# Kernel optimization log

Hardware: AMD Instinct MI355X
Metric: run time of the kernel (lower is better)

## Reference

```python
import jax, jax.numpy as jnp
import numpy as np

N = 50000   # nodes
E = 800000  # edges (sparse adjacency nnz)
FI = 256    # input feature dim
FO = 64     # output feature dim per head
H = 8       # attention heads


def setup_inputs() -> dict:
    key = jax.random.key(0)
    ks = jax.random.split(key, 6)
    x = jax.random.normal(ks[0], (N, FI), dtype=jnp.float32)
    W = jax.random.normal(ks[1], (H, FI, FO), dtype=jnp.float32) * 0.05
    a = jax.random.normal(ks[2], (H, FO), dtype=jnp.float32) * 0.05
    b = jax.random.normal(ks[3], (H, FO), dtype=jnp.float32) * 0.05
    rows = jax.random.randint(ks[4], (E,), 0, N, dtype=jnp.int32)
    cols = jax.random.randint(ks[5], (E,), 0, N, dtype=jnp.int32)
    return {"x": x, "W": W, "a": a, "b": b, "rows": rows, "cols": cols}


def reference(x, W, a, b, rows, cols):
    # SparseGAT forward: per head linear -> edge scores -> sparse row softmax
    # -> sparse aggregation -> bias; heads averaged then ReLU.
    n = x.shape[0]
    h = W.shape[0]
    NEG_SLOPE = 0.2  # tf.nn.leaky_relu default alpha
    acc = None
    for i in range(h):  # small fixed loop over heads
        t = x @ W[i]                                   # [N, FO]
        aw = t @ a[i]                                  # [N]
        e = jax.nn.leaky_relu(aw[rows] + aw[cols], NEG_SLOPE)   # [E]
        # sparse softmax per row (segment softmax, numerically stable)
        m = jax.ops.segment_max(e, rows, num_segments=n)        # [N]
        ex = jnp.exp(e - m[rows])                                # [E]
        den = jax.ops.segment_sum(ex, rows, num_segments=n)      # [N]
        coef = ex / den[rows]                                    # [E]
        # sparse matmul: sum_j coef_ij * t_j
        agg = jax.ops.segment_sum(coef[:, None] * t[cols], rows, num_segments=n)
        agg = agg + b[i]
        acc = agg if acc is None else acc + agg
    return jax.nn.relu(acc / h)
```

## Files before the change

kernel.cpp:

```cpp
#include <hip/hip_runtime.h>
#include <hip/hip_bf16.h>


#define FI 256
#define FO 64
#define NH 8
#define FC 512
#define BM 128

typedef _Float16 f16x8 __attribute__((ext_vector_type(8)));
typedef float f32x16 __attribute__((ext_vector_type(16)));
typedef float f32x8 __attribute__((ext_vector_type(8)));
typedef float f32x4 __attribute__((ext_vector_type(4)));

__global__ __launch_bounds__(256)
void p1_wconv(const float* __restrict__ W, _Float16* __restrict__ Wth) {
  int idx = blockIdx.x * 256 + threadIdx.x;
  if (idx >= NH * FO * FI) return;
  int k = idx & (FI - 1);
  int f = (idx >> 8) & (FO - 1);
  int h = idx >> 14;
  Wth[idx] = (_Float16)W[((size_t)h * FI + k) * FO + f];
}

__global__ __launch_bounds__(512)
void k1_v2(const float* __restrict__ x, const _Float16* __restrict__ Wth,
           const float* __restrict__ a, _Float16* __restrict__ Th2,
           float* __restrict__ aw, int N) {
  __shared__ _Float16 smem[BM * 136];
  auto Xs = reinterpret_cast<_Float16(*)[136]>(smem);
  auto Tt = reinterpret_cast<_Float16(*)[512]>(smem);
  const int bm = blockIdx.x * BM;
  const int t = threadIdx.x;
  const int w = t >> 6;
  const int lane = t & 63;
  const int l31 = lane & 31;
  const int kh = (lane >> 5) * 8;
  const _Float16* Wh = Wth + (size_t)w * (FO * FI);

  f32x16 acc[4][2];
  #pragma unroll
  for (int mr = 0; mr < 4; ++mr)
    #pragma unroll
    for (int wc = 0; wc < 2; ++wc) acc[mr][wc] = (f32x16)0.0f;

  #pragma unroll
  for (int k0 = 0; k0 < 2; ++k0) {
    if (k0) __syncthreads();
    #pragma unroll
    for (int r = 0; r < 8; ++r) {
      int i = t + r * 512;
      int row = i >> 5;
      int q = i & 31;
      float4 v = make_float4(0.f, 0.f, 0.f, 0.f);
      if (bm + row < N)
        v = reinterpret_cast<const float4*>(&x[(size_t)(bm + row) * FI + k0 * 128])[q];
      _Float16 o[4] = {(_Float16)v.x, (_Float16)v.y, (_Float16)v.z, (_Float16)v.w};
      *reinterpret_cast<uint2*>(&Xs[row][q * 4]) = *reinterpret_cast<uint2*>(o);
    }
    __syncthreads();
    #pragma unroll
    for (int kk = 0; kk < 8; ++kk) {
      f16x8 af[4], bf[2];
      #pragma unroll
      for (int mr = 0; mr < 4; ++mr)
        af[mr] = *reinterpret_cast<const f16x8*>(&Xs[mr * 32 + l31][kk * 16 + kh]);
      #pragma unroll
      for (int wc = 0; wc < 2; ++wc)
        bf[wc] = *reinterpret_cast<const f16x8*>(
            &Wh[(size_t)(wc * 32 + l31) * FI + k0 * 128 + kk * 16 + kh]);
      #pragma unroll
      for (int mr = 0; mr < 4; ++mr)
        #pragma unroll
        for (int wc = 0; wc < 2; ++wc)
          acc[mr][wc] =
              __builtin_amdgcn_mfma_f32_32x32x16_f16(af[mr], bf[wc], acc[mr][wc], 0, 0, 0);
    }
  }

  const float av0 = a[w * FO + l31], av1 = a[w * FO + 32 + l31];
  #pragma unroll
  for (int mr = 0; mr < 4; ++mr)
    #pragma unroll
    for (int reg = 0; reg < 16; ++reg) {
      float s = acc[mr][0][reg] * av0 + acc[mr][1][reg] * av1;
      #pragma unroll
      for (int off = 1; off < 32; off <<= 1) s += __shfl_xor(s, off);
      if (l31 == 0) {
        int rl = mr * 32 + (reg & 3) + 8 * (reg >> 2) + 4 * (lane >> 5);
        if (bm + rl < N) aw[(size_t)(bm + rl) * NH + w] = s;
      }
    }

  #pragma unroll
  for (int ch = 0; ch < 4; ++ch) {
    __syncthreads();
    #pragma unroll
    for (int wc = 0; wc < 2; ++wc) {
      const int f = wc * 32 + l31;
      #pragma unroll
      for (int reg = 0; reg < 16; ++reg) {
        int rl = (reg & 3) + 8 * (reg >> 2) + 4 * (lane >> 5);
        Tt[rl][f * NH + w] = (_Float16)acc[ch][wc][reg];
      }
    }
    __syncthreads();
    #pragma unroll
    for (int r = 0; r < 4; ++r) {
      int i = t + r * 512;
      int row = i >> 6, q = i & 63;
      int grow = bm + ch * 32 + row;
      if (grow < N)
        *reinterpret_cast<uint4*>(&Th2[(size_t)grow * FC + q * 8]) =
            *reinterpret_cast<const uint4*>(&Tt[row][q * 8]);
    }
  }
}

__global__ __launch_bounds__(256)
void b1_hist(const int* __restrict__ rows, int* __restrict__ deg, int E) {
  int e = blockIdx.x * 256 + threadIdx.x;
  if (e < E) atomicAdd(&deg[rows[e]], 1);
}

__global__ __launch_bounds__(256)
void b2a_blocksum(const int* __restrict__ deg, int* __restrict__ blocksums, int N) {
  __shared__ int red[256];
  const int t = threadIdx.x;
  const int base = blockIdx.x * 1024 + t * 4;
  int s = 0;
  #pragma unroll
  for (int j = 0; j < 4; ++j) { int i = base + j; if (i < N) s += deg[i]; }
  red[t] = s;
  __syncthreads();
  for (int off = 128; off; off >>= 1) {
    if (t < off) red[t] += red[t + off];
    __syncthreads();
  }
  if (t == 0) blocksums[blockIdx.x] = red[0];
}

__global__ __launch_bounds__(64)
void b2b_scanblocks(int* __restrict__ blocksums, int nb,
                    int* __restrict__ row_start, int N, int E) {
  const int lane = threadIdx.x;
  int carry = 0;
  for (int base = 0; base < nb; base += 64) {
    int i = base + lane;
    int v = (i < nb) ? blocksums[i] : 0;
    int inc = v;
    #pragma unroll
    for (int off = 1; off < 64; off <<= 1) {
      int t = __shfl_up(inc, off);
      if (lane >= off) inc += t;
    }
    if (i < nb) blocksums[i] = inc - v + carry;
    carry += __shfl(inc, 63);
  }
  if (lane == 0) row_start[N] = E;
}

__global__ __launch_bounds__(256)
void b2c_rescan(const int* __restrict__ deg, const int* __restrict__ blocksums,
                int* __restrict__ row_start, int* __restrict__ cursor, int N) {
  __shared__ int ts[256];
  const int t = threadIdx.x;
  const int base = blockIdx.x * 1024 + t * 4;
  int v[4]; int s = 0;
  #pragma unroll
  for (int j = 0; j < 4; ++j) { int i = base + j; v[j] = (i < N) ? deg[i] : 0; s += v[j]; }
  ts[t] = s;
  __syncthreads();
  for (int off = 1; off < 256; off <<= 1) {
    int add = (t >= off) ? ts[t - off] : 0;
    __syncthreads();
    ts[t] += add;
    __syncthreads();
  }
  int run = blocksums[blockIdx.x] + ts[t] - s;
  #pragma unroll
  for (int j = 0; j < 4; ++j) {
    int i = base + j;
    if (i < N) { row_start[i] = run; cursor[i] = run; run += v[j]; }
  }
}

__global__ __launch_bounds__(256)
void b3_scatter(const int* __restrict__ rows, const int* __restrict__ cols,
                int* __restrict__ cursor, int* __restrict__ colperm, int E) {
  int e = blockIdx.x * 256 + threadIdx.x;
  if (e >= E) return;
  int pos = atomicAdd(&cursor[rows[e]], 1);
  colperm[pos] = cols[e];
}

__global__ __launch_bounds__(256)
void k4_fused(const int* __restrict__ row_start, const int* __restrict__ colperm,
              const float* __restrict__ aw, const _Float16* __restrict__ Th2,
              const float* __restrict__ b, float* __restrict__ out, int N) {
  __shared__ float exs[16][132];
  const int lane16 = threadIdx.x & 15;
  const int g      = threadIdx.x >> 4;
  const int gbase  = threadIdx.x & 48;
  const int r = blockIdx.x * 16 + g;
  if (r >= N) return;
  float* exg = &exs[g][0];

  const int s0 = row_start[r], s1 = row_start[r + 1];
  f32x8 awr = *reinterpret_cast<const f32x8*>(&aw[(size_t)r * NH]);

  float facc[4][NH] = {};
  float dacc[NH] = {};

  for (int base = s0; base < s1; base += 16) {
    const int mm = min(16, s1 - base);
    const bool valid = lane16 < mm;
    int c_l = valid ? colperm[base + lane16] : 0;

    f32x8 awc = *reinterpret_cast<const f32x8*>(&aw[(size_t)c_l * NH]);
    #pragma unroll
    for (int h = 0; h < NH; ++h) {
      float s = awr[h] + awc[h];
      float lr = s > 0.f ? s : 0.2f * s;
      float e = valid ? __expf(lr) : 0.f;
      dacc[h] += e;
      exg[lane16 * NH + h] = e;
    }

    int cj = __shfl(c_l, gbase);
    const _Float16* tp = Th2 + (size_t)cj * FC + lane16 * NH;
    f16x8 A0 = *reinterpret_cast<const f16x8*>(tp);
    f16x8 A1 = *reinterpret_cast<const f16x8*>(tp + 128);
    f16x8 A2 = *reinterpret_cast<const f16x8*>(tp + 256);
    f16x8 A3 = *reinterpret_cast<const f16x8*>(tp + 384);
    for (int j = 0; j < mm; ++j) {
      f16x8 B0, B1, B2, B3;
      if (j + 1 < mm) {
        int cn = __shfl(c_l, gbase + j + 1);
        const _Float16* tq = Th2 + (size_t)cn * FC + lane16 * NH;
        B0 = *reinterpret_cast<const f16x8*>(tq);
        B1 = *reinterpret_cast<const f16x8*>(tq + 128);
        B2 = *reinterpret_cast<const f16x8*>(tq + 256);
        B3 = *reinterpret_cast<const f16x8*>(tq + 384);
      }
      f32x4 e0 = *reinterpret_cast<const f32x4*>(&exg[j * NH]);
      f32x4 e1 = *reinterpret_cast<const f32x4*>(&exg[j * NH + 4]);
      #pragma unroll
      for (int h = 0; h < 4; ++h) {
        facc[0][h]     = fmaf(e0[h], (float)A0[h],     facc[0][h]);
        facc[1][h]     = fmaf(e0[h], (float)A1[h],     facc[1][h]);
        facc[2][h]     = fmaf(e0[h], (float)A2[h],     facc[2][h]);
        facc[3][h]     = fmaf(e0[h], (float)A3[h],     facc[3][h]);
        facc[0][h + 4] = fmaf(e1[h], (float)A0[h + 4], facc[0][h + 4]);
        facc[1][h + 4] = fmaf(e1[h], (float)A1[h + 4], facc[1][h + 4]);
        facc[2][h + 4] = fmaf(e1[h], (float)A2[h + 4], facc[2][h + 4]);
        facc[3][h + 4] = fmaf(e1[h], (float)A3[h + 4], facc[3][h + 4]);
      }
      A0 = B0; A1 = B1; A2 = B2; A3 = B3;
    }
  }

  #pragma unroll
  for (int h = 0; h < NH; ++h) {
    #pragma unroll
    for (int off = 1; off < 16; off <<= 1)
      dacc[h] += __shfl_xor(dacc[h], off);
  }

  float rden[NH];
  #pragma unroll
  for (int h = 0; h < NH; ++h) rden[h] = dacc[h] > 0.f ? 1.0f / dacc[h] : 0.f;

  #pragma unroll
  for (int q = 0; q < 4; ++q) {
    const int f = q * 16 + lane16;
    float sb = 0.f;
    #pragma unroll
    for (int h = 0; h < NH; ++h) sb += b[h * FO + f];
    float v = 0.f;
    #pragma unroll
    for (int h = 0; h < NH; ++h) v += facc[q][h] * rden[h];
    v = (v + sb) * 0.125f;
    out[(size_t)r * FO + f] = v > 0.f ? v : 0.f;
  }
}

extern "C" void kernel_launch(void* const* d_in, const int* in_sizes, int n_in,
                              void* d_out, int out_size, void* d_ws, size_t ws_size,
                              hipStream_t stream) {
  const float* x    = (const float*)d_in[0];
  const float* W    = (const float*)d_in[1];
  const float* a    = (const float*)d_in[2];
  const float* b    = (const float*)d_in[3];
  const int*   rows = (const int*)d_in[4];
  const int*   cols = (const int*)d_in[5];
  const int N = in_sizes[0] / FI;
  const int E = in_sizes[4];

  char* p = (char*)d_ws;
  _Float16* Th2      = (_Float16*)p;  p += (size_t)N * FC * sizeof(_Float16);
  _Float16* Wth      = (_Float16*)p;  p += (size_t)NH * FO * FI * sizeof(_Float16);
  float*    aw       = (float*)p;     p += (size_t)N * NH * sizeof(float);
  int*      deg      = (int*)p;       p += (size_t)N * sizeof(int);
  int*      row_start= (int*)p;       p += (size_t)(N + 4) * sizeof(int);
  int*      cursor   = (int*)p;       p += (size_t)N * sizeof(int);
  int*      colperm  = (int*)p;       p += (size_t)E * sizeof(int);
  int*      blocksums= (int*)p;       p += 64 * sizeof(int);
  float*    out = (float*)d_out;

  const int nb = (N + 1023) / 1024;

  hipMemsetAsync(deg, 0, (size_t)N * sizeof(int), stream);
  b1_hist<<<(E + 255) / 256, 256, 0, stream>>>(rows, deg, E);
  b2a_blocksum<<<nb, 256, 0, stream>>>(deg, blocksums, N);
  b2b_scanblocks<<<1, 64, 0, stream>>>(blocksums, nb, row_start, N, E);
  b2c_rescan<<<nb, 256, 0, stream>>>(deg, blocksums, row_start, cursor, N);
  b3_scatter<<<(E + 255) / 256, 256, 0, stream>>>(rows, cols, cursor, colperm, E);

  p1_wconv<<<(NH * FO * FI + 255) / 256, 256, 0, stream>>>(W, Wth);
  k1_v2<<<(N + BM - 1) / BM, 512, 0, stream>>>(x, Wth, a, Th2, aw, N);

  k4_fused<<<(N + 15) / 16, 256, 0, stream>>>(row_start, colperm, aw, Th2, b, out, N);
}
```

Baseline: 292.6 us.

## Pipeline two neighbor rows per step, keep edge weights in registers via shuffles

The aggregation kernel now keeps the attention exponentials in registers, packs them as half2 and broadcasts them with shuffles, so the shared-memory staging buffer is gone. The inner gather loop prefetches two neighbor feature rows per iteration instead of one, which doubles memory-level parallelism. The kernel also becomes a grid-stride loop over 16-row tiles with half as many blocks. In exchange it uses more registers for the doubled buffers, adds shuffle traffic, and rounds the softmax numerators to fp16 before accumulation.

```diff
diff --git a/kernel.cpp b/kernel.cpp
--- a/kernel.cpp
+++ b/kernel.cpp
@@ -1,5 +1,6 @@
 #include <hip/hip_runtime.h>
 #include <hip/hip_bf16.h>
+#include <hip/hip_fp16.h>
 
 
 #define FI 256
@@ -198,90 +199,118 @@
 void k4_fused(const int* __restrict__ row_start, const int* __restrict__ colperm,
               const float* __restrict__ aw, const _Float16* __restrict__ Th2,
               const float* __restrict__ b, float* __restrict__ out, int N) {
-  __shared__ float exs[16][132];
   const int lane16 = threadIdx.x & 15;
-  const int g      = threadIdx.x >> 4;
   const int gbase  = threadIdx.x & 48;
-  const int r = blockIdx.x * 16 + g;
-  if (r >= N) return;
-  float* exg = &exs[g][0];
-
-  const int s0 = row_start[r], s1 = row_start[r + 1];
-  f32x8 awr = *reinterpret_cast<const f32x8*>(&aw[(size_t)r * NH]);
-
-  float facc[4][NH] = {};
-  float dacc[NH] = {};
-
-  for (int base = s0; base < s1; base += 16) {
-    const int mm = min(16, s1 - base);
-    const bool valid = lane16 < mm;
-    int c_l = valid ? colperm[base + lane16] : 0;
-
-    f32x8 awc = *reinterpret_cast<const f32x8*>(&aw[(size_t)c_l * NH]);
+  const int ntiles = (N + 15) / 16;
+
+  for (int tile = blockIdx.x; tile < ntiles; tile += gridDim.x) {
+    const int r = tile * 16 + (threadIdx.x >> 4);
+    if (r >= N) continue;
+
+    const int s0 = row_start[r], s1 = row_start[r + 1];
+    f32x8 awr = *reinterpret_cast<const f32x8*>(&aw[(size_t)r * NH]);
+
+    float facc[4][NH] = {};
+    float dacc[NH] = {};
+
+    for (int base = s0; base < s1; base += 16) {
+      const int mm = min(16, s1 - base);
+      const bool valid = lane16 < mm;
+      int c_l = valid ? colperm[base + lane16] : 0;
+
+      f32x8 awc = *reinterpret_cast<const f32x8*>(&aw[(size_t)c_l * NH]);
+      float ex[NH];
+      uint32_t pk[4];
+      #pragma unroll
+      for (int h = 0; h < NH; ++h) {
+        float s = awr[h] + awc[h];
+        float lr = s > 0.f ? s : 0.2f * s;
+        ex[h] = valid ? __expf(lr) : 0.f;
+        dacc[h] += ex[h];
+      }
+      #pragma unroll
+      for (int q = 0; q < 4; ++q) {
+        __half2 h2 = __floats2half2_rn(ex[2 * q], ex[2 * q + 1]);
+        pk[q] = *reinterpret_cast<uint32_t*>(&h2);
+      }
+
+      f16x8 A0[4], A1[4], B0[4], B1[4];
+      {
+        int c0 = __shfl(c_l, gbase + 0);
+        int c1 = __shfl(c_l, gbase + 1);
+        const _Float16* t0 = Th2 + (size_t)c0 * FC + lane16 * NH;
+        const _Float16* t1 = Th2 + (size_t)c1 * FC + lane16 * NH;
+        #pragma unroll
+        for (int q = 0; q < 4; ++q) {
+          A0[q] = *reinterpret_cast<const f16x8*>(t0 + q * 128);
+          A1[q] = *reinterpret_cast<const f16x8*>(t1 + q * 128);
+        }
+      }
+      for (int j = 0; j < mm; j += 2) {
+        if (j + 2 < mm) {
+          int c0 = __shfl(c_l, gbase + j + 2);
+          int c1 = __shfl(c_l, gbase + j + 3);
+          const _Float16* t0 = Th2 + (size_t)c0 * FC + lane16 * NH;
+          const _Float16* t1 = Th2 + (size_t)c1 * FC + lane16 * NH;
+          #pragma unroll
+          for (int q = 0; q < 4; ++q) {
+            B0[q] = *reinterpret_cast<const f16x8*>(t0 + q * 128);
+            B1[q] = *reinterpret_cast<const f16x8*>(t1 + q * 128);
+          }
+        }
+        float e0[NH], e1[NH];
+        #pragma unroll
+        for (int q = 0; q < 4; ++q) {
+          int p = __shfl((int)pk[q], gbase + j);
+          float2 f2 = __half22float2(*reinterpret_cast<__half2*>(&p));
+          e0[2 * q] = f2.x; e0[2 * q + 1] = f2.y;
+        }
+        #pragma unroll
+        for (int q = 0; q < 4; ++q) {
+          int p = __shfl((int)pk[q], gbase + j + 1);
+          float2 f2 = __half22float2(*reinterpret_cast<__half2*>(&p));
+          e1[2 * q] = f2.x; e1[2 * q + 1] = f2.y;
+        }
+        #pragma unroll
+        for (int q = 0; q < 4; ++q)
+          #pragma unroll
+          for (int h = 0; h < NH; ++h)
+            facc[q][h] = fmaf(e0[h], (float)A0[q][h], facc[q][h]);
+        if (j + 1 < mm) {
+          #pragma unroll
+          for (int q = 0; q < 4; ++q)
+            #pragma unroll
+            for (int h = 0; h < NH; ++h)
+              facc[q][h] = fmaf(e1[h], (float)A1[q][h], facc[q][h]);
+        }
+        #pragma unroll
+        for (int q = 0; q < 4; ++q) { A0[q] = B0[q]; A1[q] = B1[q]; }
+      }
+    }
+
     #pragma unroll
     for (int h = 0; h < NH; ++h) {
-      float s = awr[h] + awc[h];
-      float lr = s > 0.f ? s : 0.2f * s;
-      float e = valid ? __expf(lr) : 0.f;
-      dacc[h] += e;
-      exg[lane16 * NH + h] = e;
-    }
-
-    int cj = __shfl(c_l, gbase);
-    const _Float16* tp = Th2 + (size_t)cj * FC + lane16 * NH;
-    f16x8 A0 = *reinterpret_cast<const f16x8*>(tp);
-    f16x8 A1 = *reinterpret_cast<const f16x8*>(tp + 128);
-    f16x8 A2 = *reinterpret_cast<const f16x8*>(tp + 256);
-    f16x8 A3 = *reinterpret_cast<const f16x8*>(tp + 384);
-    for (int j = 0; j < mm; ++j) {
-      f16x8 B0, B1, B2, B3;
-      if (j + 1 < mm) {
-        int cn = __shfl(c_l, gbase + j + 1);
-        const _Float16* tq = Th2 + (size_t)cn * FC + lane16 * NH;
-        B0 = *reinterpret_cast<const f16x8*>(tq);
-        B1 = *reinterpret_cast<const f16x8*>(tq + 128);
-        B2 = *reinterpret_cast<const f16x8*>(tq + 256);
-        B3 = *reinterpret_cast<const f16x8*>(tq + 384);
-      }
-      f32x4 e0 = *reinterpret_cast<const f32x4*>(&exg[j * NH]);
-      f32x4 e1 = *reinterpret_cast<const f32x4*>(&exg[j * NH + 4]);
-      #pragma unroll
-      for (int h = 0; h < 4; ++h) {
-        facc[0][h]     = fmaf(e0[h], (float)A0[h],     facc[0][h]);
-        facc[1][h]     = fmaf(e0[h], (float)A1[h],     facc[1][h]);
-        facc[2][h]     = fmaf(e0[h], (float)A2[h],     facc[2][h]);
-        facc[3][h]     = fmaf(e0[h], (float)A3[h],     facc[3][h]);
-        facc[0][h + 4] = fmaf(e1[h], (float)A0[h + 4], facc[0][h + 4]);
-        facc[1][h + 4] = fmaf(e1[h], (float)A1[h + 4], facc[1][h + 4]);
-        facc[2][h + 4] = fmaf(e1[h], (float)A2[h + 4], facc[2][h + 4]);
-        facc[3][h + 4] = fmaf(e1[h], (float)A3[h + 4], facc[3][h + 4]);
-      }
-      A0 = B0; A1 = B1; A2 = B2; A3 = B3;
-    }
-  }
-
-  #pragma unroll
-  for (int h = 0; h < NH; ++h) {
-    #pragma unroll
-    for (int off = 1; off < 16; off <<= 1)
-      dacc[h] += __shfl_xor(dacc[h], off);
-  }
-
-  float rden[NH];
-  #pragma unroll
-  for (int h = 0; h < NH; ++h) rden[h] = dacc[h] > 0.f ? 1.0f / dacc[h] : 0.f;
-
-  #pragma unroll
-  for (int q = 0; q < 4; ++q) {
-    const int f = q * 16 + lane16;
-    float sb = 0.f;
-    #pragma unroll
-    for (int h = 0; h < NH; ++h) sb += b[h * FO + f];
-    float v = 0.f;
-    #pragma unroll
-    for (int h = 0; h < NH; ++h) v += facc[q][h] * rden[h];
-    v = (v + sb) * 0.125f;
-    out[(size_t)r * FO + f] = v > 0.f ? v : 0.f;
+      #pragma unroll
+      for (int off = 1; off < 16; off <<= 1)
+        dacc[h] += __shfl_xor(dacc[h], off);
+    }
+
+    float rden[NH];
+    #pragma unroll
+    for (int h = 0; h < NH; ++h) rden[h] = dacc[h] > 0.f ? 1.0f / dacc[h] : 0.f;
+
+    #pragma unroll
+    for (int q = 0; q < 4; ++q) {
+      const int f = q * 16 + lane16;
+      float sb = 0.f;
+      #pragma unroll
+      for (int h = 0; h < NH; ++h) sb += b[h * FO + f];
+      float v = 0.f;
+      #pragma unroll
+      for (int h = 0; h < NH; ++h) v += facc[q][h] * rden[h];
+      v = (v + sb) * 0.125f;
+      out[(size_t)r * FO + f] = v > 0.f ? v : 0.f;
+    }
   }
 }
 
@@ -320,5 +349,7 @@
   p1_wconv<<<(NH * FO * FI + 255) / 256, 256, 0, stream>>>(W, Wth);
   k1_v2<<<(N + BM - 1) / BM, 512, 0, stream>>>(x, Wth, a, Th2, aw, N);
 
-  k4_fused<<<(N + 15) / 16, 256, 0, stream>>>(row_start, colperm, aw, Th2, b, out, N);
-}
+  const int ntiles = (N + 15) / 16;
+  const int grid4 = (ntiles + 1) / 2;
+  k4_fused<<<grid4, 256, 0, stream>>>(row_start, colperm, aw, Th2, b, out, N);
+}
```

Result: slower. 298.7 us (+2.1%).

## Sort rows by degree for load-balanced aggregation and shuffle exp weights

Applied to the files above, without the earlier changes.

Builds a degree histogram during the prefix scan, then counting-sorts the rows by degree into a row_order array. The aggregation kernel processes rows in that order, so the 16-lane groups sharing a wave have similar edge counts and less divergence. The shared-memory staging of exp weights is replaced by register shuffles, and the one-step prefetch of the next neighbor row is removed. This adds two small kernels and an extra indirection, loses contiguous output and row_start access, and may expose gather latency now that prefetching is gone.

```diff
diff --git a/kernel.cpp b/kernel.cpp
--- a/kernel.cpp
+++ b/kernel.cpp
@@ -1,5 +1,6 @@
 #include <hip/hip_runtime.h>
 #include <hip/hip_bf16.h>
+#include <hip/hip_fp16.h>
 
 
 #define FI 256
@@ -7,11 +8,11 @@
 #define NH 8
 #define FC 512
 #define BM 128
+#define NBIN 64
 
 typedef _Float16 f16x8 __attribute__((ext_vector_type(8)));
 typedef float f32x16 __attribute__((ext_vector_type(16)));
 typedef float f32x8 __attribute__((ext_vector_type(8)));
-typedef float f32x4 __attribute__((ext_vector_type(4)));
 
 __global__ __launch_bounds__(256)
 void p1_wconv(const float* __restrict__ W, _Float16* __restrict__ Wth) {
@@ -162,10 +163,13 @@
 
 __global__ __launch_bounds__(256)
 void b2c_rescan(const int* __restrict__ deg, const int* __restrict__ blocksums,
-                int* __restrict__ row_start, int* __restrict__ cursor, int N) {
+                int* __restrict__ row_start, int* __restrict__ cursor,
+                int* __restrict__ degcnt, int N) {
   __shared__ int ts[256];
+  __shared__ int hist[NBIN];
   const int t = threadIdx.x;
   const int base = blockIdx.x * 1024 + t * 4;
+  if (t < NBIN) hist[t] = 0;
   int v[4]; int s = 0;
   #pragma unroll
   for (int j = 0; j < 4; ++j) { int i = base + j; v[j] = (i < N) ? deg[i] : 0; s += v[j]; }
@@ -181,8 +185,13 @@
   #pragma unroll
   for (int j = 0; j < 4; ++j) {
     int i = base + j;
-    if (i < N) { row_start[i] = run; cursor[i] = run; run += v[j]; }
-  }
+    if (i < N) {
+      row_start[i] = run; cursor[i] = run; run += v[j];
+      atomicAdd(&hist[min(v[j], NBIN - 1)], 1);
+    }
+  }
+  __syncthreads();
+  if (t < NBIN && hist[t]) atomicAdd(&degcnt[t], hist[t]);
 }
 
 __global__ __launch_bounds__(256)
@@ -194,17 +203,38 @@
   colperm[pos] = cols[e];
 }
 
+__global__ __launch_bounds__(64)
+void b4_degscan(const int* __restrict__ degcnt, int* __restrict__ degoff) {
+  const int lane = threadIdx.x;
+  int v = degcnt[lane];
+  int inc = v;
+  #pragma unroll
+  for (int off = 1; off < 64; off <<= 1) {
+    int t = __shfl_up(inc, off);
+    if (lane >= off) inc += t;
+  }
+  degoff[lane] = inc - v;
+}
+
+__global__ __launch_bounds__(256)
+void b5_roworder(const int* __restrict__ deg, int* __restrict__ degoff,
+                 int* __restrict__ row_order, int N) {
+  int i = blockIdx.x * 256 + threadIdx.x;
+  if (i >= N) return;
+  int pos = atomicAdd(&degoff[min(deg[i], NBIN - 1)], 1);
+  row_order[pos] = i;
+}
+
 __global__ __launch_bounds__(256)
 void k4_fused(const int* __restrict__ row_start, const int* __restrict__ colperm,
+              const int* __restrict__ row_order,
               const float* __restrict__ aw, const _Float16* __restrict__ Th2,
               const float* __restrict__ b, float* __restrict__ out, int N) {
-  __shared__ float exs[16][132];
   const int lane16 = threadIdx.x & 15;
-  const int g      = threadIdx.x >> 4;
   const int gbase  = threadIdx.x & 48;
-  const int r = blockIdx.x * 16 + g;
-  if (r >= N) return;
-  float* exg = &exs[g][0];
+  const int ri = blockIdx.x * 16 + (threadIdx.x >> 4);
+  if (ri >= N) return;
+  const int r = row_order[ri];
 
   const int s0 = row_start[r], s1 = row_start[r + 1];
   f32x8 awr = *reinterpret_cast<const f32x8*>(&aw[(size_t)r * NH]);
@@ -218,45 +248,30 @@
     int c_l = valid ? colperm[base + lane16] : 0;
 
     f32x8 awc = *reinterpret_cast<const f32x8*>(&aw[(size_t)c_l * NH]);
+    float ex[NH];
     #pragma unroll
     for (int h = 0; h < NH; ++h) {
       float s = awr[h] + awc[h];
       float lr = s > 0.f ? s : 0.2f * s;
-      float e = valid ? __expf(lr) : 0.f;
-      dacc[h] += e;
-      exg[lane16 * NH + h] = e;
-    }
-
-    int cj = __shfl(c_l, gbase);
-    const _Float16* tp = Th2 + (size_t)cj * FC + lane16 * NH;
-    f16x8 A0 = *reinterpret_cast<const f16x8*>(tp);
-    f16x8 A1 = *reinterpret_cast<const f16x8*>(tp + 128);
-    f16x8 A2 = *reinterpret_cast<const f16x8*>(tp + 256);
-    f16x8 A3 = *reinterpret_cast<const f16x8*>(tp + 384);
+      ex[h] = valid ? __expf(lr) : 0.f;
+      dacc[h] += ex[h];
+    }
+
     for (int j = 0; j < mm; ++j) {
-      f16x8 B0, B1, B2, B3;
-      if (j + 1 < mm) {
-        int cn = __shfl(c_l, gbase + j + 1);
-        const _Float16* tq = Th2 + (size_t)cn * FC + lane16 * NH;
-        B0 = *reinterpret_cast<const f16x8*>(tq);
-        B1 = *reinterpret_cast<const f16x8*>(tq + 128);
-        B2 = *reinterpret_cast<const f16x8*>(tq + 256);
-        B3 = *reinterpret_cast<const f16x8*>(tq + 384);
+      int cj = __shfl(c_l, gbase + j);
+      const _Float16* tp = Th2 + (size_t)cj * FC + lane16 * NH;
+      f16x8 tv0 = *reinterpret_cast<const f16x8*>(tp);
+      f16x8 tv1 = *reinterpret_cast<const f16x8*>(tp + 128);
+      f16x8 tv2 = *reinterpret_cast<const f16x8*>(tp + 256);
+      f16x8 tv3 = *reinterpret_cast<const f16x8*>(tp + 384);
+      #pragma unroll
+      for (int h = 0; h < NH; ++h) {
+        float e = __shfl(ex[h], gbase + j);
+        facc[0][h] = fmaf(e, (float)tv0[h], facc[0][h]);
+        facc[1][h] = fmaf(e, (float)tv1[h], facc[1][h]);
+        facc[2][h] = fmaf(e, (float)tv2[h], facc[2][h]);
+        facc[3][h] = fmaf(e, (float)tv3[h], facc[3][h]);
       }
-      f32x4 e0 = *reinterpret_cast<const f32x4*>(&exg[j * NH]);
-      f32x4 e1 = *reinterpret_cast<const f32x4*>(&exg[j * NH + 4]);
-      #pragma unroll
-      for (int h = 0; h < 4; ++h) {
-        facc[0][h]     = fmaf(e0[h], (float)A0[h],     facc[0][h]);
-        facc[1][h]     = fmaf(e0[h], (float)A1[h],     facc[1][h]);
-        facc[2][h]     = fmaf(e0[h], (float)A2[h],     facc[2][h]);
-        facc[3][h]     = fmaf(e0[h], (float)A3[h],     facc[3][h]);
-        facc[0][h + 4] = fmaf(e1[h], (float)A0[h + 4], facc[0][h + 4]);
-        facc[1][h + 4] = fmaf(e1[h], (float)A1[h + 4], facc[1][h + 4]);
-        facc[2][h + 4] = fmaf(e1[h], (float)A2[h + 4], facc[2][h + 4]);
-        facc[3][h + 4] = fmaf(e1[h], (float)A3[h + 4], facc[3][h + 4]);
-      }
-      A0 = B0; A1 = B1; A2 = B2; A3 = B3;
     }
   }
 
@@ -302,23 +317,29 @@
   _Float16* Wth      = (_Float16*)p;  p += (size_t)NH * FO * FI * sizeof(_Float16);
   float*    aw       = (float*)p;     p += (size_t)N * NH * sizeof(float);
   int*      deg      = (int*)p;       p += (size_t)N * sizeof(int);
+  int*      degcnt   = (int*)p;       p += NBIN * sizeof(int);
   int*      row_start= (int*)p;       p += (size_t)(N + 4) * sizeof(int);
   int*      cursor   = (int*)p;       p += (size_t)N * sizeof(int);
   int*      colperm  = (int*)p;       p += (size_t)E * sizeof(int);
   int*      blocksums= (int*)p;       p += 64 * sizeof(int);
+  int*      degoff   = (int*)p;       p += NBIN * sizeof(int);
+  int*      row_order= (int*)p;       p += (size_t)N * sizeof(int);
   float*    out = (float*)d_out;
 
   const int nb = (N + 1023) / 1024;
 
-  hipMemsetAsync(deg, 0, (size_t)N * sizeof(int), stream);
+  hipMemsetAsync(deg, 0, ((size_t)N + NBIN) * sizeof(int), stream);
   b1_hist<<<(E + 255) / 256, 256, 0, stream>>>(rows, deg, E);
   b2a_blocksum<<<nb, 256, 0, stream>>>(deg, blocksums, N);
   b2b_scanblocks<<<1, 64, 0, stream>>>(blocksums, nb, row_start, N, E);
-  b2c_rescan<<<nb, 256, 0, stream>>>(deg, blocksums, row_start, cursor, N);
+  b2c_rescan<<<nb, 256, 0, stream>>>(deg, blocksums, row_start, cursor, degcnt, N);
   b3_scatter<<<(E + 255) / 256, 256, 0, stream>>>(rows, cols, cursor, colperm, E);
+  b4_degscan<<<1, 64, 0, stream>>>(degcnt, degoff);
+  b5_roworder<<<(N + 255) / 256, 256, 0, stream>>>(deg, degoff, row_order, N);
 
   p1_wconv<<<(NH * FO * FI + 255) / 256, 256, 0, stream>>>(W, Wth);
   k1_v2<<<(N + BM - 1) / BM, 512, 0, stream>>>(x, Wth, a, Th2, aw, N);
 
-  k4_fused<<<(N + 15) / 16, 256, 0, stream>>>(row_start, colperm, aw, Th2, b, out, N);
-}
+  k4_fused<<<(N + 15) / 16, 256, 0, stream>>>(row_start, colperm, row_order,
+                                              aw, Th2, b, out, N);
+}
```

Result: slower. 435.8 us (+48.9%).
